# Performance work log

Measured on AMD Instinct MI355X. Metric: run time of the kernel, lower is better.

The kernel has to match this reference:

```python
import jax, jax.numpy as jnp
import numpy as np

H = 1024   # hidden_dim
NH = 16    # num_heads
HD = H // NH  # head_dim = 64
B, S = 2, 2048
LN_EPS = 1e-5


def setup_inputs() -> dict:
    key = jax.random.key(0)
    ks = jax.random.split(key, 5)
    scale = 1.0 / np.sqrt(H)  # xavier-ish scale for stability
    return {
        "x": jax.random.normal(ks[0], (B, S, H), dtype=jnp.float32),
        "Wq": jax.random.normal(ks[1], (H, H), dtype=jnp.float32) * scale,
        "bq": jnp.zeros((H,), jnp.float32),
        "Wk": jax.random.normal(ks[2], (H, H), dtype=jnp.float32) * scale,
        "bk": jnp.zeros((H,), jnp.float32),
        "Wv": jax.random.normal(ks[3], (H, H), dtype=jnp.float32) * scale,
        "bv": jnp.zeros((H,), jnp.float32),
        "Wo": jax.random.normal(ks[4], (H, H), dtype=jnp.float32) * scale,
        "bo": jnp.zeros((H,), jnp.float32),
        "ln_gamma": jnp.ones((H,), jnp.float32),
        "ln_beta": jnp.zeros((H,), jnp.float32),
    }


def reference(x, Wq, bq, Wk, bk, Wv, bv, Wo, bo, ln_gamma, ln_beta):
    b, s, _ = x.shape
    # QKV projections, split heads: (b, nh, s, hd)
    def split_heads(t):
        return t.reshape(b, s, NH, HD).transpose(0, 2, 1, 3)
    Q = split_heads(x @ Wq + bq)
    K = split_heads(x @ Wk + bk)
    V = split_heads(x @ Wv + bv)
    # scaled dot-product with clamp (mask=None path)
    scores = jnp.einsum('bhqd,bhkd->bhqk', Q, K) / np.sqrt(HD).astype(np.float32)
    scores = jnp.clip(scores, -10000.0, 10000.0)
    attn = jax.nn.softmax(scores, axis=-1)
    # dropout is identity in eval mode
    ctx = jnp.einsum('bhqk,bhkd->bhqd', attn, V)
    ctx = ctx.transpose(0, 2, 1, 3).reshape(b, s, H)
    out = ctx @ Wo + bo
    # residual + LayerNorm
    y = out + x
    mu = jnp.mean(y, axis=-1, keepdims=True)
    var = jnp.mean(jnp.square(y - mu), axis=-1, keepdims=True)
    y = (y - mu) * jax.lax.rsqrt(var + LN_EPS)
    return y * ln_gamma + ln_beta
```

## Files before the change

kernel.cpp:

```cpp
#include <hip/hip_runtime.h>

typedef unsigned short u16;
typedef __attribute__((ext_vector_type(8))) short shortx8;
typedef __attribute__((ext_vector_type(4))) float floatx4;
typedef __attribute__((ext_vector_type(2))) unsigned uintx2;

#define GLD16(gp, lp) __builtin_amdgcn_global_load_lds( \
    (__attribute__((address_space(1))) void*)(gp), \
    (__attribute__((address_space(3))) void*)(lp), 16, 0, 0)

__device__ __forceinline__ u16 f2bf(float f) {
  union { float f; unsigned u; } v; v.f = f;
  unsigned r = v.u + 0x7FFFu + ((v.u >> 16) & 1u);
  return (u16)(r >> 16);
}

__device__ __forceinline__ unsigned pkbf(float a, float b) {
#if __has_builtin(__builtin_amdgcn_cvt_pk_bf16_f32)
  auto r = __builtin_amdgcn_cvt_pk_bf16_f32(a, b);
  return __builtin_bit_cast(unsigned, r);
#else
  union { float f; unsigned u; } x, y; x.f = a; y.f = b;
  return __builtin_amdgcn_perm(y.u + 0x8000u, x.u + 0x8000u, 0x07060302u);
#endif
}

__global__ __launch_bounds__(256) void prep_kernel(const float* __restrict__ x,
                                                   u16* __restrict__ xb,
                                                   const float* __restrict__ Wq,
                                                   const float* __restrict__ Wk,
                                                   const float* __restrict__ Wv,
                                                   const float* __restrict__ Wo,
                                                   u16* __restrict__ Wt) {
  __shared__ u16 tile[32][33];
  int bid = blockIdx.x;
  int tid = threadIdx.x;
  if (bid < 4096) {
    int i = bid * 256 + tid;
    float4 v = ((const float4*)x)[i];
    uintx2 o;
    o.x = pkbf(v.x, v.y);
    o.y = pkbf(v.z, v.w);
    ((uintx2*)xb)[i] = o;
  } else {
    int block = bid - 4096;
    int mat = block >> 10;
    int rem = block & 1023;
    const float* W = (mat == 0) ? Wq : (mat == 1) ? Wk : (mat == 2) ? Wv : Wo;
    u16* dst = Wt + (size_t)mat * 1024 * 1024;
    int n0 = (rem & 31) * 32, k0 = (rem >> 5) * 32;
    int tx = tid & 31, ty = tid >> 5;
    for (int i = 0; i < 4; ++i)
      tile[ty + i * 8][tx] = f2bf(W[(size_t)(k0 + ty + i * 8) * 1024 + n0 + tx]);
    __syncthreads();
    for (int i = 0; i < 4; ++i)
      dst[(size_t)(n0 + ty + i * 8) * 1024 + k0 + tx] = tile[tx][ty + i * 8];
  }
}

__device__ __forceinline__ void gemm_tile_core(const u16* __restrict__ A,
                                               const u16* __restrict__ Bt,
                                               int m0, int n0,
                                               u16* As, u16* Bs,
                                               floatx4 (&acc)[4][4]) {
  const int tid = threadIdx.x;
  const int wave = tid >> 6, lane = tid & 63;
  const int lrow = lane >> 4, lcol = lane & 15;
  const int wm = wave >> 1, wn = wave & 1;

  for (int mi = 0; mi < 4; ++mi)
    for (int ni = 0; ni < 4; ++ni)
      acc[mi][ni] = (floatx4){0.f, 0.f, 0.f, 0.f};

  const u16* ap[4];
  const u16* bp[4];
  for (int l = 0; l < 4; ++l) {
    int g = (l * 4 + wave) * 64 + lane;
    int r = g >> 3, c = g & 7;
    int cc = (c ^ (r & 7)) * 8;
    ap[l] = A + (size_t)(m0 + r) * 1024 + cc;
    bp[l] = Bt + (size_t)(n0 + r) * 1024 + cc;
  }

  for (int k0 = 0; k0 < 1024; k0 += 64) {
    __syncthreads();
    for (int l = 0; l < 4; ++l) {
      GLD16(ap[l], As + (l * 4 + wave) * 512);
      GLD16(bp[l], Bs + (l * 4 + wave) * 512);
      ap[l] += 64; bp[l] += 64;
    }
    __syncthreads();
    for (int kk = 0; kk < 2; ++kk) {
      shortx8 af[4], bf[4];
      for (int mi = 0; mi < 4; ++mi) {
        int row = wm * 64 + mi * 16 + lcol;
        int gr = (kk * 4 + lrow) ^ (row & 7);
        af[mi] = *(const shortx8*)&As[row * 64 + gr * 8];
      }
      for (int ni = 0; ni < 4; ++ni) {
        int row = wn * 64 + ni * 16 + lcol;
        int gr = (kk * 4 + lrow) ^ (row & 7);
        bf[ni] = *(const shortx8*)&Bs[row * 64 + gr * 8];
      }
      for (int mi = 0; mi < 4; ++mi)
        for (int ni = 0; ni < 4; ++ni)
          acc[mi][ni] = __builtin_amdgcn_mfma_f32_16x16x32_bf16(af[mi], bf[ni], acc[mi][ni], 0, 0, 0);
    }
  }
}

__global__ __launch_bounds__(256) void qkv_gemm(const u16* __restrict__ xb,
                                                const u16* __restrict__ Wt,
                                                const float* __restrict__ bq,
                                                const float* __restrict__ bk,
                                                const float* __restrict__ bv,
                                                u16* __restrict__ Qh,
                                                u16* __restrict__ Kh,
                                                u16* __restrict__ Vth) {
  __shared__ u16 sbuf[128 * 128];
  u16* As = sbuf;
  u16* Bs = sbuf + 128 * 64;
  int m0 = blockIdx.x * 128;
  int mat = blockIdx.y >> 3;
  int n0 = (blockIdx.y & 7) * 128;
  floatx4 acc[4][4];
  gemm_tile_core(xb, Wt + (size_t)mat * 1024 * 1024, m0, n0, As, Bs, acc);

  const float* bias = (mat == 0) ? bq : (mat == 1) ? bk : bv;
  const int tid = threadIdx.x;
  const int wave = tid >> 6, lane = tid & 63;
  const int lrow = lane >> 4, lcol = lane & 15;
  const int wm = wave >> 1, wn = wave & 1;
  const float qscale = 0.18033688011f;

  if (mat < 2) {
    u16* dst = (mat == 0) ? Qh : Kh;
    float sc = (mat == 0) ? qscale : 1.0f;
    __syncthreads();
    for (int mi = 0; mi < 4; ++mi) {
      int mb = wm * 64 + mi * 16 + lrow * 4;
      for (int ni = 0; ni < 4; ++ni) {
        int n = wn * 64 + ni * 16 + lcol;
        float bval = bias[n0 + n];
        for (int r = 0; r < 4; ++r) {
          int m = mb + r;
          sbuf[m * 128 + (((n >> 3) ^ (m & 15)) * 8) + (n & 7)] =
              f2bf((acc[mi][ni][r] + bval) * sc);
        }
      }
    }
    __syncthreads();
    int row = tid >> 1, half = tid & 1;
    int m = m0 + row;
    int bb = m >> 11, s = m & 2047;
    for (int i = 0; i < 8; ++i) {
      int cg = half * 8 + i;
      int pg = cg ^ (row & 15);
      shortx8 v = *(const shortx8*)&sbuf[row * 128 + pg * 8];
      int ng = n0 + cg * 8;
      int h = ng >> 6, d = ng & 63;
      *(shortx8*)&dst[((size_t)(bb * 16 + h) * 2048 + s) * 64 + d] = v;
    }
  } else {
    for (int mi = 0; mi < 4; ++mi) {
      int mbase = m0 + wm * 64 + mi * 16 + lrow * 4;
      int bb = mbase >> 11, s = mbase & 2047;
      for (int ni = 0; ni < 4; ++ni) {
        int n = n0 + wn * 64 + ni * 16 + lcol;
        float bval = bias[n];
        int h = n >> 6, d = n & 63;
        uintx2 pk;
        pk.x = pkbf(acc[mi][ni][0] + bval, acc[mi][ni][1] + bval);
        pk.y = pkbf(acc[mi][ni][2] + bval, acc[mi][ni][3] + bval);
        *(uintx2*)&Vth[((size_t)(bb * 16 + h) * 64 + d) * 2048 + s] = pk;
      }
    }
  }
}

__global__ __launch_bounds__(256) void out_gemm(const u16* __restrict__ ctx,
                                                const u16* __restrict__ Wot,
                                                const float* __restrict__ bo,
                                                float* __restrict__ aout) {
  __shared__ u16 As[128 * 64];
  __shared__ u16 Bs[64 * 64];
  int m0 = blockIdx.x * 128;
  int n0 = blockIdx.y * 64;
  const int tid = threadIdx.x;
  const int wave = tid >> 6, lane = tid & 63;
  const int lrow = lane >> 4, lcol = lane & 15;
  const int wm = wave >> 1, wn = wave & 1;

  floatx4 acc[4][2];
  for (int mi = 0; mi < 4; ++mi)
    for (int ni = 0; ni < 2; ++ni)
      acc[mi][ni] = (floatx4){0.f, 0.f, 0.f, 0.f};

  const u16* ap[4];
  const u16* bp[2];
  for (int l = 0; l < 4; ++l) {
    int g = (l * 4 + wave) * 64 + lane;
    int r = g >> 3, c = g & 7;
    ap[l] = ctx + (size_t)(m0 + r) * 1024 + (c ^ (r & 7)) * 8;
  }
  for (int l = 0; l < 2; ++l) {
    int g = (l * 4 + wave) * 64 + lane;
    int r = g >> 3, c = g & 7;
    bp[l] = Wot + (size_t)(n0 + r) * 1024 + (c ^ (r & 7)) * 8;
  }

  for (int k0 = 0; k0 < 1024; k0 += 64) {
    __syncthreads();
    for (int l = 0; l < 4; ++l) { GLD16(ap[l], As + (l * 4 + wave) * 512); ap[l] += 64; }
    for (int l = 0; l < 2; ++l) { GLD16(bp[l], Bs + (l * 4 + wave) * 512); bp[l] += 64; }
    __syncthreads();
    for (int kk = 0; kk < 2; ++kk) {
      shortx8 af[4], bf[2];
      for (int mi = 0; mi < 4; ++mi) {
        int row = wm * 64 + mi * 16 + lcol;
        int gr = (kk * 4 + lrow) ^ (row & 7);
        af[mi] = *(const shortx8*)&As[row * 64 + gr * 8];
      }
      for (int ni = 0; ni < 2; ++ni) {
        int row = wn * 32 + ni * 16 + lcol;
        int gr = (kk * 4 + lrow) ^ (row & 7);
        bf[ni] = *(const shortx8*)&Bs[row * 64 + gr * 8];
      }
      for (int mi = 0; mi < 4; ++mi)
        for (int ni = 0; ni < 2; ++ni)
          acc[mi][ni] = __builtin_amdgcn_mfma_f32_16x16x32_bf16(af[mi], bf[ni], acc[mi][ni], 0, 0, 0);
    }
  }

  for (int mi = 0; mi < 4; ++mi) {
    int mbase = m0 + wm * 64 + mi * 16 + lrow * 4;
    for (int ni = 0; ni < 2; ++ni) {
      int n = n0 + wn * 32 + ni * 16 + lcol;
      float bval = bo[n];
      for (int r = 0; r < 4; ++r)
        aout[(size_t)(mbase + r) * 1024 + n] = acc[mi][ni][r] + bval;
    }
  }
}

__global__ __launch_bounds__(512) void attn_kernel(const u16* __restrict__ Qh,
                                                   const u16* __restrict__ Kh,
                                                   const u16* __restrict__ Vth,
                                                   u16* __restrict__ ctx) {
  __shared__ u16 QPs[128 * 64];
  __shared__ u16 Ks[2][64 * 64];
  __shared__ u16 Vs[2][64 * 64];

  int bh = blockIdx.x;
  int b = bh >> 4, h = bh & 15;
  int q0 = blockIdx.y * 128;
  int tid = threadIdx.x;
  int wave = tid >> 6, lane = tid & 63;
  int lrow = lane >> 4, lcol = lane & 15;

  const u16* Qg = Qh + ((size_t)bh * 2048 + q0) * 64;
  for (int l = 0; l < 2; ++l) {
    int g = (l * 8 + wave) * 64 + lane;
    int r = g >> 3, c = g & 7;
    GLD16(Qg + r * 64 + ((c ^ (r & 7)) * 8), QPs + (l * 8 + wave) * 512);
  }

  const u16* Kbase = Kh + (size_t)bh * 2048 * 64;
  const u16* Vbase = Vth + (size_t)bh * 64 * 2048;

  int g = wave * 64 + lane;
  int gr = g >> 3, gc = g & 7;
  int cc = (gc ^ (gr & 7)) * 8;
  const u16* kp = Kbase + (size_t)gr * 64 + cc;
  const u16* vp = Vbase + (size_t)gr * 2048 + cc;

  GLD16(kp, (u16*)Ks + wave * 512);
  GLD16(vp, (u16*)Vs + wave * 512);
  kp += 4096;
  vp += 64;
  __syncthreads();

  shortx8 qf[2];
  for (int kk = 0; kk < 2; ++kk) {
    int row = wave * 16 + lcol;
    int grr = (kk * 4 + lrow) ^ (row & 7);
    qf[kk] = *(const shortx8*)&QPs[row * 64 + grr * 8];
  }

  const short one_bf = (short)0x3F80;
  const shortx8 ones8 = {one_bf, one_bf, one_bf, one_bf, one_bf, one_bf, one_bf, one_bf};

  floatx4 o[4];
  floatx4 lacc = (floatx4){0.f, 0.f, 0.f, 0.f};
  for (int dt = 0; dt < 4; ++dt) o[dt] = (floatx4){0.f, 0.f, 0.f, 0.f};

  for (int i = 0; i < 32; ++i) {
    int cur = i & 1;
    if (i < 31) {
      GLD16(kp, (u16*)Ks + (cur ^ 1) * 4096 + wave * 512);
      GLD16(vp, (u16*)Vs + (cur ^ 1) * 4096 + wave * 512);
      kp += 4096;
      vp += 64;
    }

    floatx4 sc[4];
    for (int kt = 0; kt < 4; ++kt)
      sc[kt] = (floatx4){0.f, 0.f, 0.f, 0.f};
    for (int kk = 0; kk < 2; ++kk) {
      for (int kt = 0; kt < 4; ++kt) {
        int row = kt * 16 + lcol;
        int grr = (kk * 4 + lrow) ^ (row & 7);
        shortx8 kf = *(const shortx8*)&Ks[cur][row * 64 + grr * 8];
        sc[kt] = __builtin_amdgcn_mfma_f32_16x16x32_bf16(kf, qf[kk], sc[kt], 0, 0, 0);
      }
    }

    {
      int row = wave * 16 + lcol;
      for (int kt = 0; kt < 4; ++kt) {
        float p0 = __builtin_amdgcn_exp2f(sc[kt][0]);
        float p1 = __builtin_amdgcn_exp2f(sc[kt][1]);
        float p2 = __builtin_amdgcn_exp2f(sc[kt][2]);
        float p3 = __builtin_amdgcn_exp2f(sc[kt][3]);
        int gg = kt * 2 + (lrow >> 1);
        int addr = row * 64 + ((gg ^ (row & 7)) * 8) + (lrow & 1) * 4;
        uintx2 pk;
        pk.x = pkbf(p0, p1);
        pk.y = pkbf(p2, p3);
        *(uintx2*)&QPs[addr] = pk;
      }
    }

    for (int kk = 0; kk < 2; ++kk) {
      int prow = wave * 16 + lcol;
      int pgr = (kk * 4 + lrow) ^ (prow & 7);
      shortx8 pf = *(const shortx8*)&QPs[prow * 64 + pgr * 8];
      lacc = __builtin_amdgcn_mfma_f32_16x16x32_bf16(ones8, pf, lacc, 0, 0, 0);
      for (int dt = 0; dt < 4; ++dt) {
        int row = dt * 16 + lcol;
        int grr = (kk * 4 + lrow) ^ (row & 7);
        shortx8 vf = *(const shortx8*)&Vs[cur][row * 64 + grr * 8];
        o[dt] = __builtin_amdgcn_mfma_f32_16x16x32_bf16(vf, pf, o[dt], 0, 0, 0);
      }
    }
    __syncthreads();
  }

  {
    float inv = 1.0f / lacc[0];
    int s = q0 + wave * 16 + lcol;
    u16* dst = ctx + (size_t)(b * 2048 + s) * 1024 + h * 64 + lrow * 4;
    for (int dt = 0; dt < 4; ++dt) {
      uintx2 pk;
      pk.x = pkbf(o[dt][0] * inv, o[dt][1] * inv);
      pk.y = pkbf(o[dt][2] * inv, o[dt][3] * inv);
      *(uintx2*)(dst + dt * 16) = pk;
    }
  }
}

__global__ __launch_bounds__(256) void ln_kernel(const float* __restrict__ aout,
                                                 const float* __restrict__ x,
                                                 const float* __restrict__ gamma,
                                                 const float* __restrict__ beta,
                                                 float* __restrict__ out) {
  int row = blockIdx.x;
  int t = threadIdx.x;
  const float4* a4 = (const float4*)(aout + (size_t)row * 1024);
  const float4* x4 = (const float4*)(x + (size_t)row * 1024);
  float4 v = a4[t];
  float4 xv = x4[t];
  v.x += xv.x; v.y += xv.y; v.z += xv.z; v.w += xv.w;
  float s = v.x + v.y + v.z + v.w;
  float s2 = v.x * v.x + v.y * v.y + v.z * v.z + v.w * v.w;
  for (int off = 1; off < 64; off <<= 1) {
    s += __shfl_xor(s, off, 64);
    s2 += __shfl_xor(s2, off, 64);
  }
  __shared__ float red[8];
  int wave = t >> 6, lane = t & 63;
  if (lane == 0) { red[wave] = s; red[4 + wave] = s2; }
  __syncthreads();
  s = red[0] + red[1] + red[2] + red[3];
  s2 = red[4] + red[5] + red[6] + red[7];
  float mu = s * (1.0f / 1024.0f);
  float var = s2 * (1.0f / 1024.0f) - mu * mu;
  float rstd = rsqrtf(var + 1e-5f);
  float4 g = ((const float4*)gamma)[t];
  float4 be = ((const float4*)beta)[t];
  float4 y;
  y.x = (v.x - mu) * rstd * g.x + be.x;
  y.y = (v.y - mu) * rstd * g.y + be.y;
  y.z = (v.z - mu) * rstd * g.z + be.z;
  y.w = (v.w - mu) * rstd * g.w + be.w;
  ((float4*)(out + (size_t)row * 1024))[t] = y;
}

extern "C" void kernel_launch(void* const* d_in, const int* in_sizes, int n_in,
                              void* d_out, int out_size, void* d_ws, size_t ws_size,
                              hipStream_t stream) {
  const float* x     = (const float*)d_in[0];
  const float* Wq    = (const float*)d_in[1];
  const float* bq    = (const float*)d_in[2];
  const float* Wk    = (const float*)d_in[3];
  const float* bk    = (const float*)d_in[4];
  const float* Wv    = (const float*)d_in[5];
  const float* bv    = (const float*)d_in[6];
  const float* Wo    = (const float*)d_in[7];
  const float* bo    = (const float*)d_in[8];
  const float* gamma = (const float*)d_in[9];
  const float* beta  = (const float*)d_in[10];
  float* out = (float*)d_out;

  char* ws = (char*)d_ws;
  u16* xb   = (u16*)(ws);
  u16* Wt   = (u16*)(ws + ((size_t)8 << 20));
  u16* Qh   = (u16*)(ws + ((size_t)16 << 20));
  u16* Kh   = (u16*)(ws + ((size_t)24 << 20));
  u16* Vth  = (u16*)(ws + ((size_t)32 << 20));
  u16* ctx  = (u16*)(ws + ((size_t)40 << 20));
  float* aout = (float*)(ws + ((size_t)48 << 20));

  prep_kernel<<<8192, 256, 0, stream>>>(x, xb, Wq, Wk, Wv, Wo, Wt);
  qkv_gemm<<<dim3(32, 24), 256, 0, stream>>>(xb, Wt, bq, bk, bv, Qh, Kh, Vth);
  attn_kernel<<<dim3(32, 16), 512, 0, stream>>>(Qh, Kh, Vth, ctx);
  out_gemm<<<dim3(32, 16), 256, 0, stream>>>(ctx, Wt + (size_t)3 * 1024 * 1024, bo, aout);
  ln_kernel<<<4096, 256, 0, stream>>>(aout, x, gamma, beta, out);
}
```

Baseline: 205.5 us.

## Split attention over two key halves and merge partials in a combine kernel

Attention blocks now each cover half of the key sequence (grid z=2), writing unnormalized bf16 partial outputs and row sums that a new combine kernel adds, normalizes and writes into the context layout. This doubles the number of attention blocks to fill more CUs. V loses its double buffer to cut LDS, guarded by an explicit vmcnt wait, and the last-iteration barrier is skipped. Partial outputs are rounded to bf16 before the merge, and the extra kernel adds a launch and memory traffic. The softmax uses no running max, so adding the two halves is exact apart from rounding.

```diff
diff --git a/kernel.cpp b/kernel.cpp
--- a/kernel.cpp
+++ b/kernel.cpp
@@ -13,6 +13,10 @@
   union { float f; unsigned u; } v; v.f = f;
   unsigned r = v.u + 0x7FFFu + ((v.u >> 16) & 1u);
   return (u16)(r >> 16);
+}
+
+__device__ __forceinline__ float bf2f(unsigned lo16) {
+  union { unsigned u; float f; } t; t.u = lo16 << 16; return t.f;
 }
 
 __device__ __forceinline__ unsigned pkbf(float a, float b) {
@@ -243,17 +247,18 @@
   }
 }
 
-__global__ __launch_bounds__(512) void attn_kernel(const u16* __restrict__ Qh,
-                                                   const u16* __restrict__ Kh,
-                                                   const u16* __restrict__ Vth,
-                                                   u16* __restrict__ ctx) {
+__global__ __launch_bounds__(512, 8) void attn_kernel(const u16* __restrict__ Qh,
+                                                      const u16* __restrict__ Kh,
+                                                      const u16* __restrict__ Vth,
+                                                      u16* __restrict__ Opart,
+                                                      float* __restrict__ Lpart) {
   __shared__ u16 QPs[128 * 64];
   __shared__ u16 Ks[2][64 * 64];
-  __shared__ u16 Vs[2][64 * 64];
+  __shared__ u16 Vs[64 * 64];
 
   int bh = blockIdx.x;
-  int b = bh >> 4, h = bh & 15;
   int q0 = blockIdx.y * 128;
+  int ks = blockIdx.z;
   int tid = threadIdx.x;
   int wave = tid >> 6, lane = tid & 63;
   int lrow = lane >> 4, lcol = lane & 15;
@@ -265,8 +270,8 @@
     GLD16(Qg + r * 64 + ((c ^ (r & 7)) * 8), QPs + (l * 8 + wave) * 512);
   }
 
-  const u16* Kbase = Kh + (size_t)bh * 2048 * 64;
-  const u16* Vbase = Vth + (size_t)bh * 64 * 2048;
+  const u16* Kbase = Kh + (size_t)bh * 2048 * 64 + (size_t)ks * 1024 * 64;
+  const u16* Vbase = Vth + (size_t)bh * 64 * 2048 + ks * 1024;
 
   int g = wave * 64 + lane;
   int gr = g >> 3, gc = g & 7;
@@ -274,10 +279,10 @@
   const u16* kp = Kbase + (size_t)gr * 64 + cc;
   const u16* vp = Vbase + (size_t)gr * 2048 + cc;
 
+  GLD16(vp, (u16*)Vs + wave * 512);
   GLD16(kp, (u16*)Ks + wave * 512);
-  GLD16(vp, (u16*)Vs + wave * 512);
+  vp += 64;
   kp += 4096;
-  vp += 64;
   __syncthreads();
 
   shortx8 qf[2];
@@ -294,14 +299,14 @@
   floatx4 lacc = (floatx4){0.f, 0.f, 0.f, 0.f};
   for (int dt = 0; dt < 4; ++dt) o[dt] = (floatx4){0.f, 0.f, 0.f, 0.f};
 
-  for (int i = 0; i < 32; ++i) {
+  for (int i = 0; i < 16; ++i) {
     int cur = i & 1;
-    if (i < 31) {
-      GLD16(kp, (u16*)Ks + (cur ^ 1) * 4096 + wave * 512);
-      GLD16(vp, (u16*)Vs + (cur ^ 1) * 4096 + wave * 512);
-      kp += 4096;
+    if (i > 0) {
+      GLD16(vp, (u16*)Vs + wave * 512);
       vp += 64;
     }
+    GLD16(kp, (u16*)Ks + (cur ^ 1) * 4096 + wave * 512);
+    kp += 4096;
 
     floatx4 sc[4];
     for (int kt = 0; kt < 4; ++kt)
@@ -318,18 +323,16 @@
     {
       int row = wave * 16 + lcol;
       for (int kt = 0; kt < 4; ++kt) {
-        float p0 = __builtin_amdgcn_exp2f(sc[kt][0]);
-        float p1 = __builtin_amdgcn_exp2f(sc[kt][1]);
-        float p2 = __builtin_amdgcn_exp2f(sc[kt][2]);
-        float p3 = __builtin_amdgcn_exp2f(sc[kt][3]);
+        uintx2 pk;
+        pk.x = pkbf(__builtin_amdgcn_exp2f(sc[kt][0]), __builtin_amdgcn_exp2f(sc[kt][1]));
+        pk.y = pkbf(__builtin_amdgcn_exp2f(sc[kt][2]), __builtin_amdgcn_exp2f(sc[kt][3]));
         int gg = kt * 2 + (lrow >> 1);
         int addr = row * 64 + ((gg ^ (row & 7)) * 8) + (lrow & 1) * 4;
-        uintx2 pk;
-        pk.x = pkbf(p0, p1);
-        pk.y = pkbf(p2, p3);
         *(uintx2*)&QPs[addr] = pk;
       }
     }
+
+    asm volatile("s_waitcnt vmcnt(1)" ::: "memory");
 
     for (int kk = 0; kk < 2; ++kk) {
       int prow = wave * 16 + lcol;
@@ -339,24 +342,47 @@
       for (int dt = 0; dt < 4; ++dt) {
         int row = dt * 16 + lcol;
         int grr = (kk * 4 + lrow) ^ (row & 7);
-        shortx8 vf = *(const shortx8*)&Vs[cur][row * 64 + grr * 8];
+        shortx8 vf = *(const shortx8*)&Vs[row * 64 + grr * 8];
         o[dt] = __builtin_amdgcn_mfma_f32_16x16x32_bf16(vf, pf, o[dt], 0, 0, 0);
       }
     }
-    __syncthreads();
+    if (i < 15) __syncthreads();
   }
 
   {
-    float inv = 1.0f / lacc[0];
     int s = q0 + wave * 16 + lcol;
-    u16* dst = ctx + (size_t)(b * 2048 + s) * 1024 + h * 64 + lrow * 4;
+    size_t orow = ((size_t)(ks * 32 + bh) * 2048 + s) * 64;
     for (int dt = 0; dt < 4; ++dt) {
       uintx2 pk;
-      pk.x = pkbf(o[dt][0] * inv, o[dt][1] * inv);
-      pk.y = pkbf(o[dt][2] * inv, o[dt][3] * inv);
-      *(uintx2*)(dst + dt * 16) = pk;
-    }
-  }
+      pk.x = pkbf(o[dt][0], o[dt][1]);
+      pk.y = pkbf(o[dt][2], o[dt][3]);
+      *(uintx2*)&Opart[orow + dt * 16 + lrow * 4] = pk;
+    }
+    if (lrow == 0)
+      Lpart[(ks * 32 + bh) * 2048 + s] = lacc[0];
+  }
+}
+
+__global__ __launch_bounds__(256) void combine_kernel(const u16* __restrict__ Opart,
+                                                      const float* __restrict__ Lpart,
+                                                      u16* __restrict__ ctx) {
+  int idx = blockIdx.x * 256 + threadIdx.x;
+  int d4 = idx & 15;
+  int srow = idx >> 4;
+  uintx2 a = ((const uintx2*)Opart)[idx];
+  uintx2 b = ((const uintx2*)Opart)[idx + (1 << 20)];
+  float l = Lpart[srow] + Lpart[srow + (1 << 16)];
+  float inv = 1.0f / l;
+  float o0 = (bf2f(a.x & 0xFFFFu) + bf2f(b.x & 0xFFFFu)) * inv;
+  float o1 = (bf2f(a.x >> 16) + bf2f(b.x >> 16)) * inv;
+  float o2 = (bf2f(a.y & 0xFFFFu) + bf2f(b.y & 0xFFFFu)) * inv;
+  float o3 = (bf2f(a.y >> 16) + bf2f(b.y >> 16)) * inv;
+  int bh = srow >> 11, s = srow & 2047;
+  int bb = bh >> 4, h = bh & 15;
+  uintx2 pk;
+  pk.x = pkbf(o0, o1);
+  pk.y = pkbf(o2, o3);
+  ((uintx2*)ctx)[(size_t)(bb * 2048 + s) * 256 + h * 16 + d4] = pk;
 }
 
 __global__ __launch_bounds__(256) void ln_kernel(const float* __restrict__ aout,
@@ -420,10 +446,13 @@
   u16* Vth  = (u16*)(ws + ((size_t)32 << 20));
   u16* ctx  = (u16*)(ws + ((size_t)40 << 20));
   float* aout = (float*)(ws + ((size_t)48 << 20));
+  u16* Opart  = (u16*)(ws + ((size_t)48 << 20));
+  float* Lpart = (float*)(ws);
 
   prep_kernel<<<8192, 256, 0, stream>>>(x, xb, Wq, Wk, Wv, Wo, Wt);
   qkv_gemm<<<dim3(32, 24), 256, 0, stream>>>(xb, Wt, bq, bk, bv, Qh, Kh, Vth);
-  attn_kernel<<<dim3(32, 16), 512, 0, stream>>>(Qh, Kh, Vth, ctx);
+  attn_kernel<<<dim3(32, 16, 2), 512, 0, stream>>>(Qh, Kh, Vth, Opart, Lpart);
+  combine_kernel<<<4096, 256, 0, stream>>>(Opart, Lpart, ctx);
   out_gemm<<<dim3(32, 16), 256, 0, stream>>>(ctx, Wt + (size_t)3 * 1024 * 1024, bo, aout);
   ln_kernel<<<4096, 256, 0, stream>>>(aout, x, gamma, beta, out);
 }
```

Measured after the change: 221.8 us. 1.08x slower.
